# Optimization experiments

Hardware: AMD Instinct MI355X
Metric: run time of the kernel (lower is better)

The kernel has to match this reference:

```python
import jax, jax.numpy as jnp
import numpy as np

D_MODEL = 256; D_STATE = 128; EXPAND = 2; HEADDIM = 64
D_INNER = EXPAND * D_MODEL            # 512
NHEADS = D_INNER // HEADDIM           # 8
CONV_DIM = D_INNER + 2 * D_STATE      # 768
D_IN_PROJ = 2 * D_INNER + 2 * D_STATE + NHEADS  # 1288
KCONV = 4
BATCH = 16; SEQ = 1024; CHUNK = 64
EPS = 1e-5


def setup_inputs() -> dict:
    key = jax.random.key(0)
    ks = jax.random.split(key, 8)
    # dt_bias = inverse-softplus of dt ~ U[1e-3, 1e-1] (Mamba2 init)
    dt = jnp.exp(jax.random.uniform(ks[3], (NHEADS,), jnp.float32,
                                    np.log(1e-3), np.log(1e-1)))
    dt_bias = dt + jnp.log(-jnp.expm1(-dt))
    return {
        "u": jax.random.normal(ks[0], (BATCH, SEQ, D_MODEL), jnp.float32),
        "W_in": 0.02 * jax.random.normal(ks[1], (D_MODEL, D_IN_PROJ), jnp.float32),
        "conv_w": 0.2 * jax.random.normal(ks[2], (CONV_DIM, KCONV), jnp.float32),
        "conv_b": jnp.zeros((CONV_DIM,), jnp.float32),
        "dt_bias": dt_bias,
        "A_log": jnp.log(jax.random.uniform(ks[4], (NHEADS,), jnp.float32, 1.0, 16.0)),
        "D": jnp.ones((NHEADS,), jnp.float32),
        "norm_w": jnp.ones((D_INNER,), jnp.float32),
        "W_out": 0.02 * jax.random.normal(ks[5], (D_INNER, D_MODEL), jnp.float32),
    }


def _segsum(x):
    # x: (..., L) -> (..., L, L) lower-triangular cumulative segment sums
    L = x.shape[-1]
    c = jnp.cumsum(x, axis=-1)
    ss = c[..., :, None] - c[..., None, :]
    mask = jnp.tril(jnp.ones((L, L), bool))
    return jnp.where(mask, ss, -jnp.inf)


def _ssd(X, A, Bm, Cm, chunk):
    # Chunked SSD selective scan (Mamba2, ngroups=1).
    # X:(b,t,h,p)  A:(b,t,h)  Bm,Cm:(b,t,n)
    b, t, h, p = X.shape
    nc = t // chunk
    X = X.reshape(b, nc, chunk, h, p)
    A = A.reshape(b, nc, chunk, h).transpose(0, 3, 1, 2)   # (b,h,c,l)
    Bm = Bm.reshape(b, nc, chunk, -1)
    Cm = Cm.reshape(b, nc, chunk, -1)
    A_cs = jnp.cumsum(A, axis=-1)                          # (b,h,c,l)
    Lmat = jnp.exp(_segsum(A))                             # (b,h,c,l,l)
    # within-chunk (diagonal) contribution
    Y_diag = jnp.einsum('bcln,bcsn,bhcls,bcshp->bclhp', Cm, Bm, Lmat, X)
    # per-chunk end states
    decay_states = jnp.exp(A_cs[..., -1:] - A_cs)          # (b,h,c,l)
    states = jnp.einsum('bcln,bhcl,bclhp->bchpn', Bm, decay_states, X)
    # inter-chunk recurrence (vectorized over chunks)
    A_chunk = jnp.pad(A_cs[..., -1], ((0, 0), (0, 0), (1, 0)))
    decay_chunk = jnp.exp(_segsum(A_chunk))                # (b,h,c+1,c+1)
    states = jnp.concatenate([jnp.zeros_like(states[:, :1]), states], axis=1)
    new_states = jnp.einsum('bhzc,bchpn->bzhpn', decay_chunk, states)
    states = new_states[:, :-1]                            # state entering each chunk
    Y_off = jnp.einsum('bcln,bchpn,bhcl->bclhp', Cm, states, jnp.exp(A_cs))
    return (Y_diag + Y_off).reshape(b, t, h, p)


def reference(u, W_in, conv_w, conv_b, dt_bias, A_log, D, norm_w, W_out):
    B, T, _ = u.shape
    zxbcdt = u @ W_in                                      # (B,T,1288)
    z, xBC, dt = jnp.split(zxbcdt, [D_INNER, D_INNER + CONV_DIM], axis=-1)
    # causal depthwise conv1d, kernel KCONV
    xp = jnp.pad(xBC, ((0, 0), (KCONV - 1, 0), (0, 0)))
    kern = conv_w.T[:, None, :]                            # (K,1,C)
    xBC = jax.lax.conv_general_dilated(
        xp, kern, (1,), 'VALID',
        dimension_numbers=('NWC', 'WIO', 'NWC'), feature_group_count=CONV_DIM)
    xBC = jax.nn.silu(xBC + conv_b)
    x, Bc, Cc = jnp.split(xBC, [D_INNER, D_INNER + D_STATE], axis=-1)
    x = x.reshape(B, T, NHEADS, HEADDIM)
    dt = jax.nn.softplus(dt + dt_bias)                     # (B,T,H)
    A = -jnp.exp(A_log)                                    # (H,)
    y = _ssd(x * dt[..., None], dt * A, Bc, Cc, CHUNK)     # (B,T,H,P)
    y = y + D[:, None] * x                                 # skip term
    y = y.reshape(B, T, D_INNER)
    # gated RMSNorm: norm(y * silu(z)) * weight
    g = y * jax.nn.silu(z)
    g = g * jax.lax.rsqrt(jnp.mean(g * g, axis=-1, keepdims=True) + EPS) * norm_w
    return g @ W_out
```

## Files before the change

### kernel.cpp

```cpp
#include <hip/hip_runtime.h>
#include <hip/hip_bf16.h>
#include <math.h>

#define BATCHN  16
#define SEQ     1024
#define DMODEL  256
#define DSTATE  128
#define HEADDIM 64
#define DINNER  512
#define NHEADS  8
#define CONVDIM 768
#define DINPROJ 1288
#define ZXLD    1280
#define KCONV   4
#define NCHUNK  16
#define LCHUNK  64
#define EPSV    1e-5f
#define ROWS    (BATCHN*SEQ)

typedef __attribute__((ext_vector_type(8))) __bf16 bf16x8;
typedef __attribute__((ext_vector_type(4))) float  f32x4;

__device__ inline ushort f2bf(float f) {
    union { float f; uint32_t u; } v; v.f = f;
    uint32_t r = v.u + 0x7fff + ((v.u >> 16) & 1);
    return (ushort)(r >> 16);
}
__device__ inline float bf2f(ushort u) {
    union { uint32_t u; float f; } v; v.u = ((uint32_t)u) << 16;
    return v.f;
}

__global__ __launch_bounds__(256) void prep_k(const float* __restrict__ u,
                                              const float* __restrict__ W_in,
                                              const float* __restrict__ W_out,
                                              const float* __restrict__ dt_bias,
                                              const float* __restrict__ A_log,
                                              ushort* __restrict__ ubf,
                                              float* __restrict__ dtb,
                                              float* __restrict__ adtb,
                                              ushort* __restrict__ WtA,
                                              ushort* __restrict__ WtB) {
    __shared__ union {
        struct { float Uld[32][264]; float Ws[DMODEL][NHEADS]; } d;
        float Ts[32][33];
    } S;
    const int tid = threadIdx.x;
    if (blockIdx.x < 512) {
        #pragma unroll
        for (int j = 0; j < 8; ++j) {
            int idx = tid + j * 256;
            S.d.Ws[idx >> 3][idx & 7] = W_in[(size_t)(idx >> 3) * DINPROJ + 1280 + (idx & 7)];
        }
        const int row0 = blockIdx.x * 32;
        #pragma unroll
        for (int v = 0; v < 8; ++v) {
            int e = v * 1024 + tid * 4;
            int r = e >> 8, cc = e & 255;
            float4 x = *(const float4*)&u[(size_t)(row0 + r) * DMODEL + cc];
            *(float4*)&S.d.Uld[r][cc] = x;
            ushort t4[4];
            t4[0]=f2bf(x.x); t4[1]=f2bf(x.y); t4[2]=f2bf(x.z); t4[3]=f2bf(x.w);
            *(ushort4*)&ubf[(size_t)(row0 + r) * DMODEL + cc] = *(ushort4*)t4;
        }
        __syncthreads();
        const int row = tid >> 3, h = tid & 7;
        float acc = 0.f;
        #pragma unroll 8
        for (int k = 0; k < DMODEL; k += 4) {
            float4 uv = *(const float4*)&S.d.Uld[row][k];
            acc += uv.x * S.d.Ws[k][h] + uv.y * S.d.Ws[k+1][h]
                 + uv.z * S.d.Ws[k+2][h] + uv.w * S.d.Ws[k+3][h];
        }
        float v = acc + dt_bias[h];
        float dt = (v > 20.f) ? v : log1pf(__expf(v));
        dtb [(size_t)(row0 + row) * NHEADS + h] = dt;
        adtb[(size_t)(row0 + row) * NHEADS + h] = dt * (-__expf(A_log[h]));
    } else {
        int bid = blockIdx.x - 512;
        const float* src; ushort* dst; int K, ldsrc, nx;
        if (bid < 320) { src = W_in;  dst = WtA; K = DMODEL; ldsrc = DINPROJ; nx = 40; }
        else { bid -= 320; src = W_out; dst = WtB; K = DINNER; ldsrc = DMODEL; nx = 8; }
        const int n0 = (bid % nx) * 32, k0 = (bid / nx) * 32;
        const int tx = tid & 31, ty = tid >> 5;
        #pragma unroll
        for (int j = 0; j < 4; ++j) {
            int kl = ty * 4 + j;
            S.Ts[kl][tx] = src[(size_t)(k0 + kl) * ldsrc + n0 + tx];
        }
        __syncthreads();
        #pragma unroll
        for (int j = 0; j < 4; ++j) {
            int nl = ty * 4 + j;
            dst[(size_t)(n0 + nl) * K + k0 + tx] = f2bf(S.Ts[tx][nl]);
        }
    }
}

#define LDSW 72
#define TILEC 132
template<typename CT>
__global__ __launch_bounds__(256) void gemm_bf16(const ushort* __restrict__ A,
                                                 const ushort* __restrict__ Bt,
                                                 CT* __restrict__ C,
                                                 int M, int N, int K, int nx) {
    __shared__ ushort LB[2 * 128 * LDSW];
    ushort* As = LB;
    ushort* Bs = LB + 128 * LDSW;
    const int tid  = threadIdx.x;
    const int nwg  = gridDim.x;
    const int work = (blockIdx.x & 7) * (nwg >> 3) + (blockIdx.x >> 3);
    const int m0 = (work / nx) * 128, n0 = (work % nx) * 128;
    const int wid = tid >> 6, lane = tid & 63;
    const int wr = wid >> 1, wc = wid & 1;
    const int r = tid >> 1, kq = tid & 1;
    const int fr = lane & 15, kc = lane >> 4;

    f32x4 acc[4][4];
    #pragma unroll
    for (int i = 0; i < 4; ++i)
        #pragma unroll
        for (int j = 0; j < 4; ++j) acc[i][j] = (f32x4)0.f;

    for (int kt = 0; kt < K; kt += 64) {
        const ushort* ap = &A [(size_t)(m0 + r) * K + kt + kq * 32];
        const ushort* bp = &Bt[(size_t)(n0 + r) * K + kt + kq * 32];
        #pragma unroll
        for (int v = 0; v < 4; ++v) {
            *(uint4*)&As[r * LDSW + kq * 32 + v * 8] = *(const uint4*)(ap + v * 8);
            *(uint4*)&Bs[r * LDSW + kq * 32 + v * 8] = *(const uint4*)(bp + v * 8);
        }
        __syncthreads();
        #pragma unroll
        for (int kk = 0; kk < 2; ++kk) {
            bf16x8 af[4], bfv[4];
            #pragma unroll
            for (int i = 0; i < 4; ++i) {
                af[i]  = *(const bf16x8*)&As[(wr * 64 + i * 16 + fr) * LDSW + kk * 32 + kc * 8];
                bfv[i] = *(const bf16x8*)&Bs[(wc * 64 + i * 16 + fr) * LDSW + kk * 32 + kc * 8];
            }
            #pragma unroll
            for (int i = 0; i < 4; ++i)
                #pragma unroll
                for (int j = 0; j < 4; ++j)
                    acc[i][j] = __builtin_amdgcn_mfma_f32_16x16x32_bf16(af[i], bfv[j], acc[i][j], 0, 0, 0);
        }
        __syncthreads();
    }
    if constexpr (sizeof(CT) == 4) {
        #pragma unroll
        for (int i = 0; i < 4; ++i)
            #pragma unroll
            for (int j = 0; j < 4; ++j)
                #pragma unroll
                for (int q = 0; q < 4; ++q) {
                    int rr = m0 + wr * 64 + i * 16 + (lane >> 4) * 4 + q;
                    int cc = n0 + wc * 64 + j * 16 + (lane & 15);
                    C[(size_t)rr * N + cc] = acc[i][j][q];
                }
    } else {
        ushort (*Tile)[TILEC] = (ushort (*)[TILEC])LB;
        #pragma unroll
        for (int i = 0; i < 4; ++i)
            #pragma unroll
            for (int j = 0; j < 4; ++j)
                #pragma unroll
                for (int q = 0; q < 4; ++q)
                    Tile[wr * 64 + i * 16 + (lane >> 4) * 4 + q]
                        [wc * 64 + j * 16 + (lane & 15)] = f2bf(acc[i][j][q]);
        __syncthreads();
        #pragma unroll
        for (int it = 0; it < 8; ++it) {
            int idx = tid + it * 256;
            int rr = idx >> 4, g = idx & 15;
            *(uint4*)&C[(size_t)(m0 + rr) * N + n0 + g * 8] = *(uint4*)&Tile[rr][g * 8];
        }
    }
}

__global__ __launch_bounds__(256) void conv_silu_k(const ushort* __restrict__ zx,
                                                   const float* __restrict__ cw,
                                                   const float* __restrict__ cb,
                                                   ushort* __restrict__ out) {
    __shared__ float cws[KCONV][CONVDIM];
    __shared__ float cbs[CONVDIM];
    const int tid = threadIdx.x;
    #pragma unroll
    for (int it = 0; it < 3; ++it) {
        int i = tid + it * 256;
        cbs[i] = cb[i];
        #pragma unroll
        for (int k = 0; k < KCONV; ++k) cws[k][i] = cw[i * KCONV + k];
    }
    __syncthreads();

    const int idx = blockIdx.x * 256 + tid;
    const int cg = idx % 96, btq = idx / 96;
    const int c0 = cg * 8;
    const int bt0 = btq * 4;
    const int t0 = bt0 & (SEQ - 1);

    float wv[KCONV][8], bias[8];
    #pragma unroll
    for (int j = 0; j < 8; ++j) bias[j] = cbs[c0 + j];
    #pragma unroll
    for (int k = 0; k < KCONV; ++k) {
        float4 a = *(const float4*)&cws[k][c0];
        float4 b = *(const float4*)&cws[k][c0 + 4];
        wv[k][0] = a.x; wv[k][1] = a.y; wv[k][2] = a.z; wv[k][3] = a.w;
        wv[k][4] = b.x; wv[k][5] = b.y; wv[k][6] = b.z; wv[k][7] = b.w;
    }
    float xr[7][8];
    #pragma unroll
    for (int r = 0; r < 7; ++r) {
        int tt = t0 - 3 + r;
        if (tt >= 0) {
            uint4 v = *(const uint4*)&zx[(size_t)(bt0 - 3 + r) * ZXLD + DINNER + c0];
            const ushort* pv = (const ushort*)&v;
            #pragma unroll
            for (int j = 0; j < 8; ++j) xr[r][j] = bf2f(pv[j]);
        } else {
            #pragma unroll
            for (int j = 0; j < 8; ++j) xr[r][j] = 0.f;
        }
    }
    #pragma unroll
    for (int dt = 0; dt < 4; ++dt) {
        float acc[8];
        #pragma unroll
        for (int j = 0; j < 8; ++j) acc[j] = bias[j];
        #pragma unroll
        for (int k = 0; k < KCONV; ++k)
            #pragma unroll
            for (int j = 0; j < 8; ++j) acc[j] += xr[dt + k][j] * wv[k][j];
        ushort res[8];
        #pragma unroll
        for (int j = 0; j < 8; ++j)
            res[j] = f2bf(acc[j] / (1.f + __expf(-acc[j])));
        *(uint4*)&out[(size_t)(bt0 + dt) * CONVDIM + c0] = *(uint4*)res;
    }
}

#define SLDA 136
#define SLDB 72
__global__ __launch_bounds__(256) void ssd_mfma_k(const ushort* __restrict__ xbc,
                                                  const float* __restrict__ dtb,
                                                  const float* __restrict__ adtb,
                                                  const float* __restrict__ Dp,
                                                  ushort* __restrict__ ybuf,
                                                  ushort* __restrict__ states,
                                                  float* __restrict__ acsbuf,
                                                  float* __restrict__ chunksum) {
    const int wk = (blockIdx.x & 7) * 64 + (blockIdx.x >> 3);
    const int hgrp = wk & 1, c = (wk >> 1) & 15, b = wk >> 5;
    const int row0 = b * SEQ + c * LCHUNK;
    const int tid = threadIdx.x;
    const int lane = tid & 63, w = tid >> 6;
    const int fr = lane & 15, kc = lane >> 4;

    __shared__ union {
        struct { ushort Bs[64][SLDA]; ushort Cs[64][SLDA]; } p1;
        struct { ushort Ps[64][SLDB]; ushort Xt[64][SLDB]; ushort Xdt[64][SLDB]; } p2;
    } U;
    __shared__ ushort Btr[128][SLDB];
    __shared__ float acs4[4][64];
    __shared__ float dts[4][64];
    __shared__ float decs[4][64];

    {
        const int hh = hgrp * 4 + w;
        float v = adtb[(size_t)(row0 + lane) * NHEADS + hh];
        #pragma unroll
        for (int off = 1; off < 64; off <<= 1) {
            float t = __shfl_up(v, off);
            if (lane >= off) v += t;
        }
        acs4[w][lane] = v;
        float tot = __shfl(v, 63);
        decs[w][lane] = __expf(tot - v);
        acsbuf[(((size_t)b * NCHUNK + c) * NHEADS + hh) * LCHUNK + lane] = v;
        if (lane == 63) chunksum[((size_t)b * NCHUNK + c) * NHEADS + hh] = v;
        dts[w][lane] = dtb[(size_t)(row0 + lane) * NHEADS + hh];
    }
    for (int it = 0; it < 4; ++it) {
        int idx = tid + it * 256;
        int l = idx >> 4, ng = idx & 15;
        const ushort* rp = &xbc[(size_t)(row0 + l) * CONVDIM + DINNER];
        uint4 vb = *(const uint4*)(rp + ng * 8);
        *(uint4*)&U.p1.Bs[l][ng * 8] = vb;
        uint4 vc = *(const uint4*)(rp + DSTATE + ng * 8);
        *(uint4*)&U.p1.Cs[l][ng * 8] = vc;
        const ushort* pv = (const ushort*)&vb;
        #pragma unroll
        for (int j = 0; j < 8; ++j) Btr[ng * 8 + j][l] = pv[j];
    }
    __syncthreads();

    const int wr = w >> 1, wc = w & 1;
    f32x4 accG[2][2];
    #pragma unroll
    for (int i = 0; i < 2; ++i)
        #pragma unroll
        for (int j = 0; j < 2; ++j) accG[i][j] = (f32x4)0.f;
    #pragma unroll
    for (int kt = 0; kt < 4; ++kt) {
        bf16x8 af[2], bfv[2];
        #pragma unroll
        for (int i = 0; i < 2; ++i) af[i]  = *(const bf16x8*)&U.p1.Cs[wr*32 + i*16 + fr][kt*32 + kc*8];
        #pragma unroll
        for (int j = 0; j < 2; ++j) bfv[j] = *(const bf16x8*)&U.p1.Bs[wc*32 + j*16 + fr][kt*32 + kc*8];
        #pragma unroll
        for (int i = 0; i < 2; ++i)
            #pragma unroll
            for (int j = 0; j < 2; ++j)
                accG[i][j] = __builtin_amdgcn_mfma_f32_16x16x32_bf16(af[i], bfv[j], accG[i][j], 0, 0, 0);
    }
    __syncthreads();

    for (int hl = 0; hl < 4; ++hl) {
        const int hh = hgrp * 4 + hl;
        {
            const int p = lane;
            ushort xt[16], xdt[16];
            #pragma unroll
            for (int j = 0; j < 16; ++j) {
                int l = w * 16 + j;
                float xv = bf2f(xbc[(size_t)(row0 + l) * CONVDIM + hh * HEADDIM + p])
                           * dts[hl][l];
                xt[j]  = f2bf(xv);
                xdt[j] = f2bf(xv * decs[hl][l]);
            }
            #pragma unroll
            for (int v = 0; v < 4; ++v) {
                *(ushort4*)&U.p2.Xt [p][w*16 + v*4] = *(ushort4*)&xt[v*4];
                *(ushort4*)&U.p2.Xdt[p][w*16 + v*4] = *(ushort4*)&xdt[v*4];
            }
        }
        #pragma unroll
        for (int i = 0; i < 2; ++i)
            #pragma unroll
            for (int j = 0; j < 2; ++j)
                #pragma unroll
                for (int q = 0; q < 4; ++q) {
                    int l = wr*32 + i*16 + (lane >> 4)*4 + q;
                    int s = wc*32 + j*16 + fr;
                    float v = 0.f;
                    if (s < l)       v = accG[i][j][q] * __expf(acs4[hl][l] - acs4[hl][s]);
                    else if (s == l) v = accG[i][j][q] + Dp[hh] / dts[hl][l];
                    U.p2.Ps[l][s] = f2bf(v);
                }
        __syncthreads();
        {
            f32x4 acc[4];
            #pragma unroll
            for (int j = 0; j < 4; ++j) acc[j] = (f32x4)0.f;
            #pragma unroll
            for (int kt = 0; kt < 2; ++kt) {
                bf16x8 af = *(const bf16x8*)&U.p2.Ps[w*16 + fr][kt*32 + kc*8];
                #pragma unroll
                for (int j = 0; j < 4; ++j) {
                    bf16x8 bfv = *(const bf16x8*)&U.p2.Xt[j*16 + fr][kt*32 + kc*8];
                    acc[j] = __builtin_amdgcn_mfma_f32_16x16x32_bf16(af, bfv, acc[j], 0, 0, 0);
                }
            }
            #pragma unroll
            for (int j = 0; j < 4; ++j)
                #pragma unroll
                for (int q = 0; q < 4; ++q) {
                    int l = w*16 + (lane >> 4)*4 + q;
                    int p = j*16 + fr;
                    ybuf[(size_t)(row0 + l) * DINNER + hh * HEADDIM + p] = f2bf(acc[j][q]);
                }
        }
        {
            f32x4 acc2[4][2];
            #pragma unroll
            for (int mt = 0; mt < 4; ++mt)
                #pragma unroll
                for (int jt = 0; jt < 2; ++jt) acc2[mt][jt] = (f32x4)0.f;
            #pragma unroll
            for (int kt = 0; kt < 2; ++kt) {
                bf16x8 a4[4], b2[2];
                #pragma unroll
                for (int mt = 0; mt < 4; ++mt) a4[mt] = *(const bf16x8*)&U.p2.Xdt[mt*16 + fr][kt*32 + kc*8];
                #pragma unroll
                for (int jt = 0; jt < 2; ++jt) b2[jt] = *(const bf16x8*)&Btr[w*32 + jt*16 + fr][kt*32 + kc*8];
                #pragma unroll
                for (int mt = 0; mt < 4; ++mt)
                    #pragma unroll
                    for (int jt = 0; jt < 2; ++jt)
                        acc2[mt][jt] = __builtin_amdgcn_mfma_f32_16x16x32_bf16(a4[mt], b2[jt], acc2[mt][jt], 0, 0, 0);
            }
            ushort* sb = states + ((((size_t)b * NCHUNK + c) * NHEADS + hh) * HEADDIM) * DSTATE;
            #pragma unroll
            for (int mt = 0; mt < 4; ++mt)
                #pragma unroll
                for (int jt = 0; jt < 2; ++jt)
                    #pragma unroll
                    for (int q = 0; q < 4; ++q) {
                        int p = mt*16 + (lane >> 4)*4 + q;
                        int n = w*32 + jt*16 + fr;
                        sb[(size_t)p * DSTATE + n] = f2bf(acc2[mt][jt][q]);
                    }
        }
        __syncthreads();
    }
}

__global__ __launch_bounds__(256) void scan_k(ushort* __restrict__ states,
                                              const float* __restrict__ chunksum) {
    const int bid = blockIdx.x;
    const int pq = bid & 3, h = (bid >> 2) & 7, b = bid >> 5;
    const int tid = threadIdx.x;
    float pref[8];
    #pragma unroll
    for (int k = 0; k < 8; ++k) pref[k] = 0.f;
    for (int c = 0; c < NCHUNK; ++c) {
        ushort* base = states + (((size_t)b * NCHUNK + c) * NHEADS + h) * (HEADDIM * DSTATE)
                       + pq * 2048 + tid * 8;
        float dec = __expf(chunksum[((size_t)b * NCHUNK + c) * NHEADS + h]);
        uint4 v = *(const uint4*)base;
        const ushort* pv = (const ushort*)&v;
        ushort outv[8];
        #pragma unroll
        for (int j = 0; j < 8; ++j) {
            float cur = bf2f(pv[j]);
            outv[j] = f2bf(pref[j]);
            pref[j] = dec * pref[j] + cur;
        }
        *(uint4*)base = *(uint4*)outv;
    }
}

__global__ __launch_bounds__(256) void yoff_gate_k(const ushort* __restrict__ xbc,
                                                   const ushort* __restrict__ states,
                                                   const float* __restrict__ acsbuf,
                                                   const ushort* __restrict__ ybuf,
                                                   const ushort* __restrict__ zx,
                                                   const float* __restrict__ nw,
                                                   ushort* __restrict__ gbuf) {
    const int wk = (blockIdx.x & 7) * 64 + (blockIdx.x >> 3);
    const int half = wk & 1, c = (wk >> 1) & 15, b = wk >> 5;
    const int row0 = b * SEQ + c * LCHUNK + half * 32;
    const int tid = threadIdx.x;
    const int lane = tid & 63, w = tid >> 6;
    const int fr = lane & 15, kc = lane >> 4;
    const int rw = (w & 1) * 16;
    const int j0 = (w >> 1) * 2;
    __shared__ ushort Csh[32][SLDA];
    __shared__ ushort Ssh[64][SLDA];
    __shared__ ushort Ys[32][520];
    __shared__ float eah[32];

    #pragma unroll
    for (int it = 0; it < 2; ++it) {
        int idx = tid + it * 256;
        int l = idx >> 4, ng = idx & 15;
        *(uint4*)&Csh[l][ng * 8] =
            *(const uint4*)&xbc[(size_t)(row0 + l) * CONVDIM + DINNER + DSTATE + ng * 8];
    }
    for (int hl = 0; hl < NHEADS; ++hl) {
        __syncthreads();
        const ushort* sb = states + ((((size_t)b * NCHUNK + c) * NHEADS + hl) * HEADDIM) * DSTATE;
        #pragma unroll
        for (int it = 0; it < 4; ++it) {
            int idx = tid + it * 256;
            int p = idx >> 4, ng = idx & 15;
            *(uint4*)&Ssh[p][ng * 8] = *(const uint4*)&sb[(size_t)p * DSTATE + ng * 8];
        }
        if (tid < 32)
            eah[tid] = __expf(acsbuf[(((size_t)b * NCHUNK + c) * NHEADS + hl) * LCHUNK
                                     + half * 32 + tid]);
        __syncthreads();
        f32x4 acc[2];
        acc[0] = (f32x4)0.f; acc[1] = (f32x4)0.f;
        #pragma unroll
        for (int kt = 0; kt < 4; ++kt) {
            bf16x8 af = *(const bf16x8*)&Csh[rw + fr][kt*32 + kc*8];
            #pragma unroll
            for (int jj = 0; jj < 2; ++jj) {
                bf16x8 bfv = *(const bf16x8*)&Ssh[(j0+jj)*16 + fr][kt*32 + kc*8];
                acc[jj] = __builtin_amdgcn_mfma_f32_16x16x32_bf16(af, bfv, acc[jj], 0, 0, 0);
            }
        }
        #pragma unroll
        for (int jj = 0; jj < 2; ++jj)
            #pragma unroll
            for (int q = 0; q < 4; ++q) {
                int l = rw + (lane >> 4)*4 + q;
                int p = (j0+jj)*16 + fr;
                float val = bf2f(ybuf[(size_t)(row0 + l) * DINNER + hl * HEADDIM + p])
                            + acc[jj][q] * eah[l];
                Ys[l][hl * HEADDIM + p] = f2bf(val);
            }
    }
    __syncthreads();
    float nwv[8];
    #pragma unroll
    for (int j = 0; j < 8; ++j) nwv[j] = nw[lane * 8 + j];
    #pragma unroll
    for (int i = 0; i < 8; ++i) {
        int l = w * 8 + i;
        int row = row0 + l;
        uint4 zv = *(const uint4*)&zx[(size_t)row * ZXLD + lane * 8];
        const ushort* pz = (const ushort*)&zv;
        float g[8], ss = 0.f;
        #pragma unroll
        for (int j = 0; j < 8; ++j) {
            float y = bf2f(Ys[l][lane * 8 + j]);
            float z = bf2f(pz[j]);
            float sz = z / (1.f + __expf(-z));
            g[j] = y * sz;
            ss += g[j] * g[j];
        }
        #pragma unroll
        for (int off = 32; off; off >>= 1) ss += __shfl_xor(ss, off);
        float r = rsqrtf(ss / (float)DINNER + EPSV);
        ushort res[8];
        #pragma unroll
        for (int j = 0; j < 8; ++j) res[j] = f2bf(g[j] * r * nwv[j]);
        *(uint4*)&gbuf[(size_t)row * DINNER + lane * 8] = *(uint4*)res;
    }
}

extern "C" void kernel_launch(void* const* d_in, const int* in_sizes, int n_in,
                              void* d_out, int out_size, void* d_ws, size_t ws_size,
                              hipStream_t stream) {
    const float* u       = (const float*)d_in[0];
    const float* W_in    = (const float*)d_in[1];
    const float* conv_w  = (const float*)d_in[2];
    const float* conv_b  = (const float*)d_in[3];
    const float* dt_bias = (const float*)d_in[4];
    const float* A_log   = (const float*)d_in[5];
    const float* Dp      = (const float*)d_in[6];
    const float* norm_w  = (const float*)d_in[7];
    const float* W_out   = (const float*)d_in[8];
    float* out = (float*)d_out;

    char* p = (char*)d_ws;
    ushort* zx       = (ushort*)p; p += (size_t)ROWS * ZXLD * sizeof(ushort);
    ushort* ybuf     = (ushort*)p; p += (size_t)ROWS * DINNER * sizeof(ushort);
    ushort* gbuf     = (ushort*)p; p += (size_t)ROWS * DINNER * sizeof(ushort);
    ushort* states   = (ushort*)p; p += (size_t)BATCHN * NCHUNK * NHEADS * HEADDIM * DSTATE * sizeof(ushort);
    ushort* xbc      = (ushort*)p; p += (size_t)ROWS * CONVDIM * sizeof(ushort);
    ushort* ubf      = (ushort*)p; p += (size_t)ROWS * DMODEL * sizeof(ushort);
    float*  dtb      = (float*)p;  p += (size_t)ROWS * NHEADS  * sizeof(float);
    float*  adtb     = (float*)p;  p += (size_t)ROWS * NHEADS  * sizeof(float);
    float*  chunksum = (float*)p;  p += (size_t)BATCHN * NCHUNK * NHEADS * sizeof(float);
    float*  acsbuf   = (float*)p;  p += (size_t)BATCHN * NCHUNK * NHEADS * LCHUNK * sizeof(float);
    ushort* WtA      = (ushort*)p; p += (size_t)ZXLD * DMODEL * sizeof(ushort);
    ushort* WtB      = (ushort*)p; p += (size_t)DMODEL * DINNER * sizeof(ushort);

    prep_k<<<960, 256, 0, stream>>>(u, W_in, W_out, dt_bias, A_log,
                                    ubf, dtb, adtb, WtA, WtB);
    gemm_bf16<ushort><<<(ZXLD/128)*(ROWS/128), 256, 0, stream>>>(
        ubf, WtA, zx, ROWS, ZXLD, DMODEL, ZXLD/128);
    conv_silu_k<<<(ROWS/4)*96/256, 256, 0, stream>>>(zx, conv_w, conv_b, xbc);
    ssd_mfma_k<<<512, 256, 0, stream>>>(
        xbc, dtb, adtb, Dp, ybuf, states, acsbuf, chunksum);
    scan_k<<<BATCHN*NHEADS*4, 256, 0, stream>>>(states, chunksum);
    yoff_gate_k<<<512, 256, 0, stream>>>(
        xbc, states, acsbuf, ybuf, zx, norm_w, gbuf);
    gemm_bf16<float><<<(DMODEL/128)*(ROWS/128), 256, 0, stream>>>(
        gbuf, WtB, out, ROWS, DMODEL, DINNER, DMODEL/128);
}
```

Before: 125.4 us.

## Move intra-chunk diagonal SSD output into the tail kernel, dropping ybuf round trip

The intra-chunk diagonal term (C·Bᵀ masked with decay, times dt-scaled X) moves out of the state-computation kernel and into the tail kernel that adds the inter-chunk contribution and applies the gated RMSNorm. This removes the bf16 ybuf intermediate write and re-read through global memory and makes the states kernel lighter. In exchange, the tail kernel reloads B for the full chunk, recomputes the C·Bᵀ product, and builds P and X^T per head. This adds shared memory, LDS transposes and synchronisation there, which could reduce occupancy.

```diff
diff --git a/kernel.cpp b/kernel.cpp
--- a/kernel.cpp
+++ b/kernel.cpp
@@ -241,16 +241,13 @@
     }
 }
 
-#define SLDA 136
 #define SLDB 72
-__global__ __launch_bounds__(256) void ssd_mfma_k(const ushort* __restrict__ xbc,
-                                                  const float* __restrict__ dtb,
-                                                  const float* __restrict__ adtb,
-                                                  const float* __restrict__ Dp,
-                                                  ushort* __restrict__ ybuf,
-                                                  ushort* __restrict__ states,
-                                                  float* __restrict__ acsbuf,
-                                                  float* __restrict__ chunksum) {
+__global__ __launch_bounds__(256) void states_k(const ushort* __restrict__ xbc,
+                                                const float* __restrict__ dtb,
+                                                const float* __restrict__ adtb,
+                                                ushort* __restrict__ states,
+                                                float* __restrict__ acsbuf,
+                                                float* __restrict__ chunksum) {
     const int wk = (blockIdx.x & 7) * 64 + (blockIdx.x >> 3);
     const int hgrp = wk & 1, c = (wk >> 1) & 15, b = wk >> 5;
     const int row0 = b * SEQ + c * LCHUNK;
@@ -258,12 +255,8 @@
     const int lane = tid & 63, w = tid >> 6;
     const int fr = lane & 15, kc = lane >> 4;
 
-    __shared__ union {
-        struct { ushort Bs[64][SLDA]; ushort Cs[64][SLDA]; } p1;
-        struct { ushort Ps[64][SLDB]; ushort Xt[64][SLDB]; ushort Xdt[64][SLDB]; } p2;
-    } U;
     __shared__ ushort Btr[128][SLDB];
-    __shared__ float acs4[4][64];
+    __shared__ ushort Xdt[64][SLDB];
     __shared__ float dts[4][64];
     __shared__ float decs[4][64];
 
@@ -275,7 +268,6 @@
             float t = __shfl_up(v, off);
             if (lane >= off) v += t;
         }
-        acs4[w][lane] = v;
         float tot = __shfl(v, 63);
         decs[w][lane] = __expf(tot - v);
         acsbuf[(((size_t)b * NCHUNK + c) * NHEADS + hh) * LCHUNK + lane] = v;
@@ -285,35 +277,10 @@
     for (int it = 0; it < 4; ++it) {
         int idx = tid + it * 256;
         int l = idx >> 4, ng = idx & 15;
-        const ushort* rp = &xbc[(size_t)(row0 + l) * CONVDIM + DINNER];
-        uint4 vb = *(const uint4*)(rp + ng * 8);
-        *(uint4*)&U.p1.Bs[l][ng * 8] = vb;
-        uint4 vc = *(const uint4*)(rp + DSTATE + ng * 8);
-        *(uint4*)&U.p1.Cs[l][ng * 8] = vc;
+        uint4 vb = *(const uint4*)&xbc[(size_t)(row0 + l) * CONVDIM + DINNER + ng * 8];
         const ushort* pv = (const ushort*)&vb;
         #pragma unroll
         for (int j = 0; j < 8; ++j) Btr[ng * 8 + j][l] = pv[j];
-    }
-    __syncthreads();
-
-    const int wr = w >> 1, wc = w & 1;
-    f32x4 accG[2][2];
-    #pragma unroll
-    for (int i = 0; i < 2; ++i)
-        #pragma unroll
-        for (int j = 0; j < 2; ++j) accG[i][j] = (f32x4)0.f;
-    #pragma unroll
-    for (int kt = 0; kt < 4; ++kt) {
-        bf16x8 af[2], bfv[2];
-        #pragma unroll
-        for (int i = 0; i < 2; ++i) af[i]  = *(const bf16x8*)&U.p1.Cs[wr*32 + i*16 + fr][kt*32 + kc*8];
-        #pragma unroll
-        for (int j = 0; j < 2; ++j) bfv[j] = *(const bf16x8*)&U.p1.Bs[wc*32 + j*16 + fr][kt*32 + kc*8];
-        #pragma unroll
-        for (int i = 0; i < 2; ++i)
-            #pragma unroll
-            for (int j = 0; j < 2; ++j)
-                accG[i][j] = __builtin_amdgcn_mfma_f32_16x16x32_bf16(af[i], bfv[j], accG[i][j], 0, 0, 0);
     }
     __syncthreads();
 
@@ -321,57 +288,19 @@
         const int hh = hgrp * 4 + hl;
         {
             const int p = lane;
-            ushort xt[16], xdt[16];
+            ushort xdt[16];
             #pragma unroll
             for (int j = 0; j < 16; ++j) {
                 int l = w * 16 + j;
                 float xv = bf2f(xbc[(size_t)(row0 + l) * CONVDIM + hh * HEADDIM + p])
                            * dts[hl][l];
-                xt[j]  = f2bf(xv);
                 xdt[j] = f2bf(xv * decs[hl][l]);
             }
             #pragma unroll
-            for (int v = 0; v < 4; ++v) {
-                *(ushort4*)&U.p2.Xt [p][w*16 + v*4] = *(ushort4*)&xt[v*4];
-                *(ushort4*)&U.p2.Xdt[p][w*16 + v*4] = *(ushort4*)&xdt[v*4];
-            }
-        }
-        #pragma unroll
-        for (int i = 0; i < 2; ++i)
-            #pragma unroll
-            for (int j = 0; j < 2; ++j)
-                #pragma unroll
-                for (int q = 0; q < 4; ++q) {
-                    int l = wr*32 + i*16 + (lane >> 4)*4 + q;
-                    int s = wc*32 + j*16 + fr;
-                    float v = 0.f;
-                    if (s < l)       v = accG[i][j][q] * __expf(acs4[hl][l] - acs4[hl][s]);
-                    else if (s == l) v = accG[i][j][q] + Dp[hh] / dts[hl][l];
-                    U.p2.Ps[l][s] = f2bf(v);
-                }
-        __syncthreads();
-        {
-            f32x4 acc[4];
-            #pragma unroll
-            for (int j = 0; j < 4; ++j) acc[j] = (f32x4)0.f;
-            #pragma unroll
-            for (int kt = 0; kt < 2; ++kt) {
-                bf16x8 af = *(const bf16x8*)&U.p2.Ps[w*16 + fr][kt*32 + kc*8];
-                #pragma unroll
-                for (int j = 0; j < 4; ++j) {
-                    bf16x8 bfv = *(const bf16x8*)&U.p2.Xt[j*16 + fr][kt*32 + kc*8];
-                    acc[j] = __builtin_amdgcn_mfma_f32_16x16x32_bf16(af, bfv, acc[j], 0, 0, 0);
-                }
-            }
-            #pragma unroll
-            for (int j = 0; j < 4; ++j)
-                #pragma unroll
-                for (int q = 0; q < 4; ++q) {
-                    int l = w*16 + (lane >> 4)*4 + q;
-                    int p = j*16 + fr;
-                    ybuf[(size_t)(row0 + l) * DINNER + hh * HEADDIM + p] = f2bf(acc[j][q]);
-                }
-        }
+            for (int v = 0; v < 4; ++v)
+                *(ushort4*)&Xdt[p][w*16 + v*4] = *(ushort4*)&xdt[v*4];
+        }
+        __syncthreads();
         {
             f32x4 acc2[4][2];
             #pragma unroll
@@ -382,7 +311,7 @@
             for (int kt = 0; kt < 2; ++kt) {
                 bf16x8 a4[4], b2[2];
                 #pragma unroll
-                for (int mt = 0; mt < 4; ++mt) a4[mt] = *(const bf16x8*)&U.p2.Xdt[mt*16 + fr][kt*32 + kc*8];
+                for (int mt = 0; mt < 4; ++mt) a4[mt] = *(const bf16x8*)&Xdt[mt*16 + fr][kt*32 + kc*8];
                 #pragma unroll
                 for (int jt = 0; jt < 2; ++jt) b2[jt] = *(const bf16x8*)&Btr[w*32 + jt*16 + fr][kt*32 + kc*8];
                 #pragma unroll
@@ -432,25 +361,34 @@
     }
 }
 
-__global__ __launch_bounds__(256) void yoff_gate_k(const ushort* __restrict__ xbc,
-                                                   const ushort* __restrict__ states,
-                                                   const float* __restrict__ acsbuf,
-                                                   const ushort* __restrict__ ybuf,
-                                                   const ushort* __restrict__ zx,
-                                                   const float* __restrict__ nw,
-                                                   ushort* __restrict__ gbuf) {
+#define SLDA 136
+__global__ __launch_bounds__(256) void tail_k(const ushort* __restrict__ xbc,
+                                              const ushort* __restrict__ states,
+                                              const float* __restrict__ acsbuf,
+                                              const float* __restrict__ dtb,
+                                              const float* __restrict__ Dp,
+                                              const ushort* __restrict__ zx,
+                                              const float* __restrict__ nw,
+                                              ushort* __restrict__ gbuf) {
     const int wk = (blockIdx.x & 7) * 64 + (blockIdx.x >> 3);
     const int half = wk & 1, c = (wk >> 1) & 15, b = wk >> 5;
-    const int row0 = b * SEQ + c * LCHUNK + half * 32;
+    const int rowC0 = b * SEQ + c * LCHUNK;
+    const int row0  = rowC0 + half * 32;
     const int tid = threadIdx.x;
     const int lane = tid & 63, w = tid >> 6;
     const int fr = lane & 15, kc = lane >> 4;
-    const int rw = (w & 1) * 16;
-    const int j0 = (w >> 1) * 2;
+    const int ri = w & 1;
+    const int cj0 = (w >> 1) * 2;
+
+    __shared__ union {
+        ushort Bs [64][SLDA];
+        ushort Ssh[64][SLDA];
+    } U;
     __shared__ ushort Csh[32][SLDA];
-    __shared__ ushort Ssh[64][SLDA];
-    __shared__ ushort Ys[32][520];
-    __shared__ float eah[32];
+    __shared__ ushort Ps [32][SLDB];
+    __shared__ ushort Xt [64][SLDB];
+    __shared__ ushort Ys [32][520];
+    __shared__ float acs_s[64], dts_s[64], ea[32];
 
     #pragma unroll
     for (int it = 0; it < 2; ++it) {
@@ -459,6 +397,27 @@
         *(uint4*)&Csh[l][ng * 8] =
             *(const uint4*)&xbc[(size_t)(row0 + l) * CONVDIM + DINNER + DSTATE + ng * 8];
     }
+    #pragma unroll
+    for (int it = 0; it < 4; ++it) {
+        int idx = tid + it * 256;
+        int l = idx >> 4, ng = idx & 15;
+        *(uint4*)&U.Bs[l][ng * 8] =
+            *(const uint4*)&xbc[(size_t)(rowC0 + l) * CONVDIM + DINNER + ng * 8];
+    }
+    __syncthreads();
+
+    f32x4 accG[2];
+    accG[0] = (f32x4)0.f; accG[1] = (f32x4)0.f;
+    #pragma unroll
+    for (int kt = 0; kt < 4; ++kt) {
+        bf16x8 af = *(const bf16x8*)&Csh[ri*16 + fr][kt*32 + kc*8];
+        #pragma unroll
+        for (int jj = 0; jj < 2; ++jj) {
+            bf16x8 bfv = *(const bf16x8*)&U.Bs[(cj0+jj)*16 + fr][kt*32 + kc*8];
+            accG[jj] = __builtin_amdgcn_mfma_f32_16x16x32_bf16(af, bfv, accG[jj], 0, 0, 0);
+        }
+    }
+
     for (int hl = 0; hl < NHEADS; ++hl) {
         __syncthreads();
         const ushort* sb = states + ((((size_t)b * NCHUNK + c) * NHEADS + hl) * HEADDIM) * DSTATE;
@@ -466,32 +425,69 @@
         for (int it = 0; it < 4; ++it) {
             int idx = tid + it * 256;
             int p = idx >> 4, ng = idx & 15;
-            *(uint4*)&Ssh[p][ng * 8] = *(const uint4*)&sb[(size_t)p * DSTATE + ng * 8];
-        }
-        if (tid < 32)
-            eah[tid] = __expf(acsbuf[(((size_t)b * NCHUNK + c) * NHEADS + hl) * LCHUNK
-                                     + half * 32 + tid]);
-        __syncthreads();
-        f32x4 acc[2];
-        acc[0] = (f32x4)0.f; acc[1] = (f32x4)0.f;
+            *(uint4*)&U.Ssh[p][ng * 8] = *(const uint4*)&sb[(size_t)p * DSTATE + ng * 8];
+        }
+        if (tid < 64) {
+            acs_s[tid] = acsbuf[(((size_t)b * NCHUNK + c) * NHEADS + hl) * LCHUNK + tid];
+            dts_s[tid] = dtb[(size_t)(rowC0 + tid) * NHEADS + hl];
+        }
+        __syncthreads();
+        {
+            int l = tid >> 2, pg = tid & 3;
+            float dt_l = dts_s[l];
+            #pragma unroll
+            for (int h2 = 0; h2 < 2; ++h2) {
+                uint4 xv4 = *(const uint4*)&xbc[(size_t)(rowC0 + l) * CONVDIM
+                                                + hl * HEADDIM + h2 * 32 + pg * 8];
+                const ushort* pv = (const ushort*)&xv4;
+                #pragma unroll
+                for (int j = 0; j < 8; ++j)
+                    Xt[h2*32 + pg*8 + j][l] = f2bf(bf2f(pv[j]) * dt_l);
+            }
+        }
+        const float Dh = Dp[hl];
+        #pragma unroll
+        for (int jj = 0; jj < 2; ++jj)
+            #pragma unroll
+            for (int q = 0; q < 4; ++q) {
+                int ll = ri*16 + (lane >> 4)*4 + q;
+                int lg = half*32 + ll;
+                int s  = (cj0+jj)*16 + fr;
+                float v = 0.f;
+                if (s < lg)       v = accG[jj][q] * __expf(acs_s[lg] - acs_s[s]);
+                else if (s == lg) v = accG[jj][q] + Dh / dts_s[lg];
+                Ps[ll][s] = f2bf(v);
+            }
+        if (tid < 32) ea[tid] = __expf(acs_s[half*32 + tid]);
+        __syncthreads();
+        f32x4 accD[2], accO[2];
+        accD[0] = (f32x4)0.f; accD[1] = (f32x4)0.f;
+        accO[0] = (f32x4)0.f; accO[1] = (f32x4)0.f;
+        #pragma unroll
+        for (int kt = 0; kt < 2; ++kt) {
+            bf16x8 af = *(const bf16x8*)&Ps[ri*16 + fr][kt*32 + kc*8];
+            #pragma unroll
+            for (int jj = 0; jj < 2; ++jj) {
+                bf16x8 bfv = *(const bf16x8*)&Xt[(cj0+jj)*16 + fr][kt*32 + kc*8];
+                accD[jj] = __builtin_amdgcn_mfma_f32_16x16x32_bf16(af, bfv, accD[jj], 0, 0, 0);
+            }
+        }
         #pragma unroll
         for (int kt = 0; kt < 4; ++kt) {
-            bf16x8 af = *(const bf16x8*)&Csh[rw + fr][kt*32 + kc*8];
+            bf16x8 af = *(const bf16x8*)&Csh[ri*16 + fr][kt*32 + kc*8];
             #pragma unroll
             for (int jj = 0; jj < 2; ++jj) {
-                bf16x8 bfv = *(const bf16x8*)&Ssh[(j0+jj)*16 + fr][kt*32 + kc*8];
-                acc[jj] = __builtin_amdgcn_mfma_f32_16x16x32_bf16(af, bfv, acc[jj], 0, 0, 0);
+                bf16x8 bfv = *(const bf16x8*)&U.Ssh[(cj0+jj)*16 + fr][kt*32 + kc*8];
+                accO[jj] = __builtin_amdgcn_mfma_f32_16x16x32_bf16(af, bfv, accO[jj], 0, 0, 0);
             }
         }
         #pragma unroll
         for (int jj = 0; jj < 2; ++jj)
             #pragma unroll
             for (int q = 0; q < 4; ++q) {
-                int l = rw + (lane >> 4)*4 + q;
-                int p = (j0+jj)*16 + fr;
-                float val = bf2f(ybuf[(size_t)(row0 + l) * DINNER + hl * HEADDIM + p])
-                            + acc[jj][q] * eah[l];
-                Ys[l][hl * HEADDIM + p] = f2bf(val);
+                int ll = ri*16 + (lane >> 4)*4 + q;
+                int p  = (cj0+jj)*16 + fr;
+                Ys[ll][hl * HEADDIM + p] = f2bf(accD[jj][q] + accO[jj][q] * ea[ll]);
             }
     }
     __syncthreads();
@@ -539,7 +535,6 @@
 
     char* p = (char*)d_ws;
     ushort* zx       = (ushort*)p; p += (size_t)ROWS * ZXLD * sizeof(ushort);
-    ushort* ybuf     = (ushort*)p; p += (size_t)ROWS * DINNER * sizeof(ushort);
     ushort* gbuf     = (ushort*)p; p += (size_t)ROWS * DINNER * sizeof(ushort);
     ushort* states   = (ushort*)p; p += (size_t)BATCHN * NCHUNK * NHEADS * HEADDIM * DSTATE * sizeof(ushort);
     ushort* xbc      = (ushort*)p; p += (size_t)ROWS * CONVDIM * sizeof(ushort);
@@ -556,11 +551,9 @@
     gemm_bf16<ushort><<<(ZXLD/128)*(ROWS/128), 256, 0, stream>>>(
         ubf, WtA, zx, ROWS, ZXLD, DMODEL, ZXLD/128);
     conv_silu_k<<<(ROWS/4)*96/256, 256, 0, stream>>>(zx, conv_w, conv_b, xbc);
-    ssd_mfma_k<<<512, 256, 0, stream>>>(
-        xbc, dtb, adtb, Dp, ybuf, states, acsbuf, chunksum);
+    states_k<<<512, 256, 0, stream>>>(xbc, dtb, adtb, states, acsbuf, chunksum);
     scan_k<<<BATCHN*NHEADS*4, 256, 0, stream>>>(states, chunksum);
-    yoff_gate_k<<<512, 256, 0, stream>>>(
-        xbc, states, acsbuf, ybuf, zx, norm_w, gbuf);
+    tail_k<<<512, 256, 0, stream>>>(xbc, states, acsbuf, dtb, Dp, zx, norm_w, gbuf);
     gemm_bf16<float><<<(DMODEL/128)*(ROWS/128), 256, 0, stream>>>(
         gbuf, WtB, out, ROWS, DMODEL, DINNER, DMODEL/128);
 }
```

Result: slower. 128.5 us (+2.5%).

## Fuse output projection GEMM into gated RMSNorm kernel

Applied to the files above, without the earlier changes.

The gated-norm result is now kept in shared memory and multiplied by W_out directly inside yoff_gate_k with MFMA, writing the final fp32 output. This removes the gbuf write/read round trip through global memory and one kernel launch. In exchange each 32-row block re-reads the whole W_out (256x512 bf16) from global/L2 without LDS staging, and the GEMM runs on small 32-row tiles with lower MFMA reuse.

```diff
diff --git a/kernel.cpp b/kernel.cpp
--- a/kernel.cpp
+++ b/kernel.cpp
@@ -99,10 +99,9 @@
 
 #define LDSW 72
 #define TILEC 132
-template<typename CT>
 __global__ __launch_bounds__(256) void gemm_bf16(const ushort* __restrict__ A,
                                                  const ushort* __restrict__ Bt,
-                                                 CT* __restrict__ C,
+                                                 ushort* __restrict__ C,
                                                  int M, int N, int K, int nx) {
     __shared__ ushort LB[2 * 128 * LDSW];
     ushort* As = LB;
@@ -147,34 +146,21 @@
         }
         __syncthreads();
     }
-    if constexpr (sizeof(CT) == 4) {
-        #pragma unroll
-        for (int i = 0; i < 4; ++i)
-            #pragma unroll
-            for (int j = 0; j < 4; ++j)
-                #pragma unroll
-                for (int q = 0; q < 4; ++q) {
-                    int rr = m0 + wr * 64 + i * 16 + (lane >> 4) * 4 + q;
-                    int cc = n0 + wc * 64 + j * 16 + (lane & 15);
-                    C[(size_t)rr * N + cc] = acc[i][j][q];
-                }
-    } else {
-        ushort (*Tile)[TILEC] = (ushort (*)[TILEC])LB;
-        #pragma unroll
-        for (int i = 0; i < 4; ++i)
-            #pragma unroll
-            for (int j = 0; j < 4; ++j)
-                #pragma unroll
-                for (int q = 0; q < 4; ++q)
-                    Tile[wr * 64 + i * 16 + (lane >> 4) * 4 + q]
-                        [wc * 64 + j * 16 + (lane & 15)] = f2bf(acc[i][j][q]);
-        __syncthreads();
-        #pragma unroll
-        for (int it = 0; it < 8; ++it) {
-            int idx = tid + it * 256;
-            int rr = idx >> 4, g = idx & 15;
-            *(uint4*)&C[(size_t)(m0 + rr) * N + n0 + g * 8] = *(uint4*)&Tile[rr][g * 8];
-        }
+    ushort (*Tile)[TILEC] = (ushort (*)[TILEC])LB;
+    #pragma unroll
+    for (int i = 0; i < 4; ++i)
+        #pragma unroll
+        for (int j = 0; j < 4; ++j)
+            #pragma unroll
+            for (int q = 0; q < 4; ++q)
+                Tile[wr * 64 + i * 16 + (lane >> 4) * 4 + q]
+                    [wc * 64 + j * 16 + (lane & 15)] = f2bf(acc[i][j][q]);
+    __syncthreads();
+    #pragma unroll
+    for (int it = 0; it < 8; ++it) {
+        int idx = tid + it * 256;
+        int rr = idx >> 4, g = idx & 15;
+        *(uint4*)&C[(size_t)(m0 + rr) * N + n0 + g * 8] = *(uint4*)&Tile[rr][g * 8];
     }
 }
 
@@ -438,7 +424,8 @@
                                                    const ushort* __restrict__ ybuf,
                                                    const ushort* __restrict__ zx,
                                                    const float* __restrict__ nw,
-                                                   ushort* __restrict__ gbuf) {
+                                                   const ushort* __restrict__ WtB,
+                                                   float* __restrict__ out) {
     const int wk = (blockIdx.x & 7) * 64 + (blockIdx.x >> 3);
     const int half = wk & 1, c = (wk >> 1) & 15, b = wk >> 5;
     const int row0 = b * SEQ + c * LCHUNK + half * 32;
@@ -519,7 +506,43 @@
         ushort res[8];
         #pragma unroll
         for (int j = 0; j < 8; ++j) res[j] = f2bf(g[j] * r * nwv[j]);
-        *(uint4*)&gbuf[(size_t)row * DINNER + lane * 8] = *(uint4*)res;
+        *(ushort4*)&Ys[l][lane * 8]     = *(ushort4*)&res[0];
+        *(ushort4*)&Ys[l][lane * 8 + 4] = *(ushort4*)&res[4];
+    }
+    __syncthreads();
+    {
+        const int cj0 = w * 4;
+        f32x4 accO[2][4];
+        #pragma unroll
+        for (int ri = 0; ri < 2; ++ri)
+            #pragma unroll
+            for (int j = 0; j < 4; ++j) accO[ri][j] = (f32x4)0.f;
+        for (int kt = 0; kt < 16; ++kt) {
+            bf16x8 af[2], bfv[4];
+            #pragma unroll
+            for (int ri = 0; ri < 2; ++ri)
+                af[ri] = *(const bf16x8*)&Ys[ri*16 + fr][kt*32 + kc*8];
+            #pragma unroll
+            for (int j = 0; j < 4; ++j) {
+                int n = (cj0 + j) * 16 + fr;
+                bfv[j] = *(const bf16x8*)&WtB[(size_t)n * DINNER + kt*32 + kc*8];
+            }
+            #pragma unroll
+            for (int ri = 0; ri < 2; ++ri)
+                #pragma unroll
+                for (int j = 0; j < 4; ++j)
+                    accO[ri][j] = __builtin_amdgcn_mfma_f32_16x16x32_bf16(af[ri], bfv[j], accO[ri][j], 0, 0, 0);
+        }
+        #pragma unroll
+        for (int ri = 0; ri < 2; ++ri)
+            #pragma unroll
+            for (int j = 0; j < 4; ++j)
+                #pragma unroll
+                for (int q = 0; q < 4; ++q) {
+                    int rr = row0 + ri*16 + (lane >> 4)*4 + q;
+                    int cc = (cj0 + j)*16 + fr;
+                    out[(size_t)rr * DMODEL + cc] = accO[ri][j][q];
+                }
     }
 }
 
@@ -540,7 +563,6 @@
     char* p = (char*)d_ws;
     ushort* zx       = (ushort*)p; p += (size_t)ROWS * ZXLD * sizeof(ushort);
     ushort* ybuf     = (ushort*)p; p += (size_t)ROWS * DINNER * sizeof(ushort);
-    ushort* gbuf     = (ushort*)p; p += (size_t)ROWS * DINNER * sizeof(ushort);
     ushort* states   = (ushort*)p; p += (size_t)BATCHN * NCHUNK * NHEADS * HEADDIM * DSTATE * sizeof(ushort);
     ushort* xbc      = (ushort*)p; p += (size_t)ROWS * CONVDIM * sizeof(ushort);
     ushort* ubf      = (ushort*)p; p += (size_t)ROWS * DMODEL * sizeof(ushort);
@@ -553,14 +575,12 @@
 
     prep_k<<<960, 256, 0, stream>>>(u, W_in, W_out, dt_bias, A_log,
                                     ubf, dtb, adtb, WtA, WtB);
-    gemm_bf16<ushort><<<(ZXLD/128)*(ROWS/128), 256, 0, stream>>>(
+    gemm_bf16<<<(ZXLD/128)*(ROWS/128), 256, 0, stream>>>(
         ubf, WtA, zx, ROWS, ZXLD, DMODEL, ZXLD/128);
     conv_silu_k<<<(ROWS/4)*96/256, 256, 0, stream>>>(zx, conv_w, conv_b, xbc);
     ssd_mfma_k<<<512, 256, 0, stream>>>(
         xbc, dtb, adtb, Dp, ybuf, states, acsbuf, chunksum);
     scan_k<<<BATCHN*NHEADS*4, 256, 0, stream>>>(states, chunksum);
     yoff_gate_k<<<512, 256, 0, stream>>>(
-        xbc, states, acsbuf, ybuf, zx, norm_w, gbuf);
-    gemm_bf16<float><<<(DMODEL/128)*(ROWS/128), 256, 0, stream>>>(
-        gbuf, WtB, out, ROWS, DMODEL, DINNER, DMODEL/128);
-}
+        xbc, states, acsbuf, ybuf, zx, norm_w, WtB, out);
+}
```

Result: faster. 120.5 us (-3.9%).
